# Optimization experiments

Hardware: AMD Instinct MI355X
Metric: run time of the kernel (lower is better)

Reference implementation:

```python
import jax, jax.numpy as jnp
import numpy as np

N_NODES = 50000
N_EDGES = 50000  # per-node attention scores are used as per-hyperedge weights => M == N
IN_CH = 128
OUT_CH = 128
NNZ = 800000


def setup_inputs() -> dict:
    key = jax.random.key(0)
    k = jax.random.split(key, 7)
    x = jax.random.normal(k[0], (N_NODES, IN_CH), dtype=jnp.float32)
    node_idx = jax.random.randint(k[1], (NNZ,), 0, N_NODES)
    edge_idx = jax.random.randint(k[2], (NNZ,), 0, N_EDGES)
    hyperedge_index = jnp.stack([node_idx, edge_idx]).astype(jnp.int64)
    s_in = 1.0 / np.sqrt(IN_CH)
    attn_w = jax.random.uniform(k[3], (1, IN_CH), minval=-s_in, maxval=s_in, dtype=jnp.float32)
    attn_b = jax.random.uniform(k[4], (1,), minval=-s_in, maxval=s_in, dtype=jnp.float32)
    lin_w = jax.random.uniform(k[5], (OUT_CH, IN_CH), minval=-s_in, maxval=s_in, dtype=jnp.float32)
    bias = jax.random.uniform(k[6], (OUT_CH,), minval=-s_in, maxval=s_in, dtype=jnp.float32)
    return {"x": x, "hyperedge_index": hyperedge_index,
            "attn_w": attn_w, "attn_b": attn_b, "lin_w": lin_w, "bias": bias}


def reference(x, hyperedge_index, attn_w, attn_b, lin_w, bias):
    # x: [N, C_in]; hyperedge_index: [2, nnz] (row 0: node ids, row 1: hyperedge ids)
    node_idx = hyperedge_index[0]
    edge_idx = hyperedge_index[1]
    N = x.shape[0]
    M = N_EDGES

    # edge_weight = sigmoid(attn(x)) -> used as hyperedge_weight (per-edge, M == N)
    w = jax.nn.sigmoid(x @ attn_w.T + attn_b)[:, 0]            # [M]

    xl = x @ lin_w.T                                           # [N, C_out]

    # D_v = sum of incident hyperedge weights per node; D^{-1} with inf -> 0
    D = jax.ops.segment_sum(w[edge_idx], node_idx, num_segments=N)
    Dinv = jnp.where(D > 0, 1.0 / D, 0.0)                      # [N]

    # B_e = hyperedge degree; B^{-1} with inf -> 0
    ones = jnp.ones(edge_idx.shape, dtype=x.dtype)
    Bdeg = jax.ops.segment_sum(ones, edge_idx, num_segments=M)
    Binv = jnp.where(Bdeg > 0, 1.0 / Bdeg, 0.0)                # [M]

    # node -> hyperedge: message = B_e^{-1} * x_j, aggregated at edge e
    msg = Binv[edge_idx][:, None] * xl[node_idx]               # [nnz, C_out]
    e_feat = jax.ops.segment_sum(msg, edge_idx, num_segments=M)

    # hyperedge -> node: message = D_v^{-1} * e_feat, aggregated at node v
    out = jax.ops.segment_sum(e_feat[edge_idx], node_idx, num_segments=N)
    out = Dinv[:, None] * out

    return out + bias
```

## Files before the change

### kernel.cpp

```cpp
#include <hip/hip_runtime.h>
#include <math.h>

#define CH 128
#define CAP 64
#define RSB 9
#define RS  (1 << RSB)
#define CAPB 10240
#define PB 2048
#define SUB 16
#define IDS 32

typedef __attribute__((ext_vector_type(8))) short bf16x8;
typedef __attribute__((ext_vector_type(4))) float f32x4;

__device__ __forceinline__ unsigned short f2bf(float f) {
    union { float f; unsigned u; } v; v.f = f;
    unsigned r = v.u + 0x7FFF + ((v.u >> 16) & 1);
    return (unsigned short)(r >> 16);
}
__device__ __forceinline__ float bflo(unsigned u) {
    union { unsigned u; float f; } v; v.u = u << 16; return v.f;
}
__device__ __forceinline__ float bfhi(unsigned u) {
    union { unsigned u; float f; } v; v.u = u & 0xFFFF0000u; return v.f;
}
__device__ __forceinline__ unsigned pack2bf(float a, float b) {
    return (unsigned)f2bf(a) | ((unsigned)f2bf(b) << 16);
}

__global__ __launch_bounds__(256) void fused_main(const float* __restrict__ x,
                                                  const float* __restrict__ attn_w,
                                                  const float* __restrict__ attn_b,
                                                  const float* __restrict__ lw,
                                                  unsigned short* __restrict__ xl,
                                                  float* __restrict__ w,
                                                  int nStrips,
                                                  const int* __restrict__ nidx,
                                                  const int* __restrict__ eidx,
                                                  int* __restrict__ binCnt,
                                                  unsigned int* __restrict__ binData,
                                                  int nnz, int nbd, int SB) {
    __shared__ unsigned short wl[128 * 136];
    __shared__ float awl[128];
    if ((int)blockIdx.x < SB) {
        int* hist = (int*)wl;
        int* base = ((int*)wl) + 256;
        int nbt = 2 * nbd;
        for (int i = threadIdx.x; i < nbt; i += 256) hist[i] = 0;
        __syncthreads();
        int k0 = blockIdx.x * PB + threadIdx.x;
        int vv[8], ee[8], sE[8], sN[8];
#pragma unroll
        for (int u = 0; u < 8; ++u) {
            int k = k0 + u * 256;
            if (k < nnz) {
                int v = nidx[k], e = eidx[k];
                vv[u] = v; ee[u] = e;
                sE[u] = atomicAdd(&hist[e >> RSB], 1);
                sN[u] = atomicAdd(&hist[nbd + (v >> RSB)], 1);
            } else vv[u] = -1;
        }
        __syncthreads();
        for (int i = threadIdx.x; i < nbt; i += 256)
            if (hist[i]) base[i] = atomicAdd(&binCnt[i], hist[i]);
        __syncthreads();
#pragma unroll
        for (int u = 0; u < 8; ++u) {
            if (vv[u] < 0) continue;
            int bE = ee[u] >> RSB;
            int bN = nbd + (vv[u] >> RSB);
            int iE = min(base[bE] + sE[u], CAPB - 1);
            int iN = min(base[bN] + sN[u], CAPB - 1);
            binData[(size_t)bE * CAPB + iE] = ((unsigned)ee[u] << 16) | (unsigned)vv[u];
            binData[(size_t)bN * CAPB + iN] = ((unsigned)vv[u] << 16) | (unsigned)ee[u];
        }
        return;
    }
    int tid = threadIdx.x;
    for (int i = tid; i < 2048; i += 256) {
        float4 vlo = ((const float4*)lw)[2 * i];
        float4 vhi = ((const float4*)lw)[2 * i + 1];
        int4 dst;
        dst.x = (int)pack2bf(vlo.x, vlo.y);
        dst.y = (int)pack2bf(vlo.z, vlo.w);
        dst.z = (int)pack2bf(vhi.x, vhi.y);
        dst.w = (int)pack2bf(vhi.z, vhi.w);
        *(int4*)(wl + (i >> 4) * 136 + (i & 15) * 8) = dst;
    }
    if (tid < 128) awl[tid] = attn_w[tid];
    float ab = attn_b[0];
    __syncthreads();
    int gb = blockIdx.x - SB;
    int wid = (gb << 2) | (tid >> 6);
    int lane = tid & 63;
    int m = lane & 15, quad = lane >> 4;
    int nWaves = ((int)gridDim.x - SB) << 2;
    for (int s = wid; s < nStrips; s += nWaves) {
        int r0 = s << 4;
        const float* xr = x + (size_t)(r0 + m) * CH + quad * 8;
        float att = 0.f;
        bf16x8 a0, a1, a2, a3;
#define LOAD_FRAG(AFRAG, F)                                                   \
        {                                                                     \
            float4 lo = *(const float4*)(xr + (F) * 32);                      \
            float4 hi = *(const float4*)(xr + (F) * 32 + 4);                  \
            const float* ap = &awl[(F) * 32 + quad * 8];                      \
            att += lo.x * ap[0] + lo.y * ap[1] + lo.z * ap[2] + lo.w * ap[3]  \
                 + hi.x * ap[4] + hi.y * ap[5] + hi.z * ap[6] + hi.w * ap[7]; \
            union { int4 i; bf16x8 v; } pk;                                   \
            pk.i.x = (int)pack2bf(lo.x, lo.y);                                \
            pk.i.y = (int)pack2bf(lo.z, lo.w);                                \
            pk.i.z = (int)pack2bf(hi.x, hi.y);                                \
            pk.i.w = (int)pack2bf(hi.z, hi.w);                                \
            AFRAG = pk.v;                                                     \
        }
        LOAD_FRAG(a0, 0)
        LOAD_FRAG(a1, 1)
        LOAD_FRAG(a2, 2)
        LOAD_FRAG(a3, 3)
#undef LOAD_FRAG
        att += __shfl_xor(att, 16, 64);
        att += __shfl_xor(att, 32, 64);
        if (quad == 0) w[r0 + m] = 1.0f / (1.0f + expf(-(att + ab)));
        unsigned short* xrow = xl + (size_t)(r0 + m) * CH + quad * 4;
#pragma unroll
        for (int c0 = 0; c0 < 128; c0 += 16) {
            const unsigned short* wr = wl + (c0 + m) * 136 + quad * 8;
            f32x4 acc = {0.f, 0.f, 0.f, 0.f};
            acc = __builtin_amdgcn_mfma_f32_16x16x32_bf16(*(const bf16x8*)(wr),      a0, acc, 0, 0, 0);
            acc = __builtin_amdgcn_mfma_f32_16x16x32_bf16(*(const bf16x8*)(wr + 32), a1, acc, 0, 0, 0);
            acc = __builtin_amdgcn_mfma_f32_16x16x32_bf16(*(const bf16x8*)(wr + 64), a2, acc, 0, 0, 0);
            acc = __builtin_amdgcn_mfma_f32_16x16x32_bf16(*(const bf16x8*)(wr + 96), a3, acc, 0, 0, 0);
            uint2 o;
            o.x = pack2bf(acc[0], acc[1]);
            o.y = pack2bf(acc[2], acc[3]);
            *(uint2*)(xrow + c0) = o;
        }
    }
}

__global__ __launch_bounds__(512, 8) void edge_agg(const int* __restrict__ binCnt,
                                                   const unsigned int* __restrict__ binData,
                                                   const unsigned short* __restrict__ xl,
                                                   unsigned short* __restrict__ ef, int M) {
    __shared__ unsigned short bucket[IDS * CAP];
    __shared__ int cl[IDS];
    int cb = blockIdx.x >> 4;
    int sr = blockIdx.x & (SUB - 1);
    int idBase = (cb << RSB) + (sr << 5);
    if (threadIdx.x < IDS) cl[threadIdx.x] = 0;
    __syncthreads();
    int n = min(binCnt[cb], CAPB);
    const unsigned int* src = binData + (size_t)cb * CAPB;
#define SCAN1(E) { int lid = (int)((E) >> 16) - idBase;                        \
                   if ((unsigned)lid < IDS) {                                  \
                       int r = atomicAdd(&cl[lid], 1);                         \
                       bucket[(lid << 6) + min(r, CAP - 1)] =                  \
                           (unsigned short)((E) & 0xFFFFu); } }
    for (int i0 = (int)threadIdx.x << 2; i0 < n; i0 += 2048) {
        if (i0 + 4 <= n) {
            uint4 e4 = *(const uint4*)(src + i0);
            SCAN1(e4.x) SCAN1(e4.y) SCAN1(e4.z) SCAN1(e4.w)
        } else {
            for (int i = i0; i < n; ++i) { unsigned int e1 = src[i]; SCAN1(e1) }
        }
    }
    __syncthreads();
    int wid = threadIdx.x >> 6, lane = threadIdx.x & 63;
    int half = lane >> 5, hl = lane & 31;
    for (int li = wid; li < IDS; li += 8) {
        int gid = idBase + li;
        if (gid >= M) break;
        int deg = cl[li];
        int dl = min(deg, CAP);
        const unsigned short* col = bucket + (li << 6);
        float4 acc = {0.f, 0.f, 0.f, 0.f};
        int npair = dl >> 1;
        int j = 0;
#define ROW(MID) { uint2 u = *(const uint2*)(xl + (size_t)(MID) * CH + 4 * hl); \
                   acc.x += bflo(u.x); acc.y += bfhi(u.x);                      \
                   acc.z += bflo(u.y); acc.w += bfhi(u.y); }
        for (; j + 4 <= npair; j += 4) {
            int m0 = col[2 * j + half];
            int m1 = col[2 * j + 2 + half];
            int m2 = col[2 * j + 4 + half];
            int m3 = col[2 * j + 6 + half];
            ROW(m0) ROW(m1) ROW(m2) ROW(m3)
        }
        for (; j < npair; ++j) { int m0 = col[2 * j + half]; ROW(m0) }
        if ((dl & 1) && half == 0) { int m0 = col[dl - 1]; ROW(m0) }
#undef ROW
        acc.x += __shfl_xor(acc.x, 32, 64);
        acc.y += __shfl_xor(acc.y, 32, 64);
        acc.z += __shfl_xor(acc.z, 32, 64);
        acc.w += __shfl_xor(acc.w, 32, 64);
        if (half == 0) {
            float binv = deg > 0 ? 1.0f / (float)deg : 0.0f;
            uint2 o;
            o.x = pack2bf(acc.x * binv, acc.y * binv);
            o.y = pack2bf(acc.z * binv, acc.w * binv);
            *(uint2*)(ef + (size_t)gid * CH + 4 * hl) = o;
        }
    }
}

__global__ __launch_bounds__(512, 8) void node_agg(const int* __restrict__ binCnt,
                                                   const unsigned int* __restrict__ binData,
                                                   const unsigned short* __restrict__ ef,
                                                   const float* __restrict__ w,
                                                   const float* __restrict__ bias,
                                                   float* __restrict__ out, int N) {
    __shared__ unsigned short bucket[IDS * CAP];
    __shared__ int cl[IDS];
    int cb = blockIdx.x >> 4;
    int sr = blockIdx.x & (SUB - 1);
    int idBase = (cb << RSB) + (sr << 5);
    if (threadIdx.x < IDS) cl[threadIdx.x] = 0;
    __syncthreads();
    int n = min(binCnt[cb], CAPB);
    const unsigned int* src = binData + (size_t)cb * CAPB;
    for (int i0 = (int)threadIdx.x << 2; i0 < n; i0 += 2048) {
        if (i0 + 4 <= n) {
            uint4 e4 = *(const uint4*)(src + i0);
            SCAN1(e4.x) SCAN1(e4.y) SCAN1(e4.z) SCAN1(e4.w)
        } else {
            for (int i = i0; i < n; ++i) { unsigned int e1 = src[i]; SCAN1(e1) }
        }
    }
#undef SCAN1
    __syncthreads();
    int wid = threadIdx.x >> 6, lane = threadIdx.x & 63;
    int half = lane >> 5, hl = lane & 31;
    for (int li = wid; li < IDS; li += 8) {
        int gid = idBase + li;
        if (gid >= N) break;
        int deg = cl[li];
        int dl = min(deg, CAP);
        const unsigned short* col = bucket + (li << 6);
        float4 acc = {0.f, 0.f, 0.f, 0.f};
        float ds = 0.f;
        int npair = dl >> 1;
        int j = 0;
#define ROW(MID) { uint2 u = *(const uint2*)(ef + (size_t)(MID) * CH + 4 * hl); \
                   ds += w[MID];                                                \
                   acc.x += bflo(u.x); acc.y += bfhi(u.x);                      \
                   acc.z += bflo(u.y); acc.w += bfhi(u.y); }
        for (; j + 4 <= npair; j += 4) {
            int m0 = col[2 * j + half];
            int m1 = col[2 * j + 2 + half];
            int m2 = col[2 * j + 4 + half];
            int m3 = col[2 * j + 6 + half];
            ROW(m0) ROW(m1) ROW(m2) ROW(m3)
        }
        for (; j < npair; ++j) { int m0 = col[2 * j + half]; ROW(m0) }
        if ((dl & 1) && half == 0) { int m0 = col[dl - 1]; ROW(m0) }
#undef ROW
        acc.x += __shfl_xor(acc.x, 32, 64);
        acc.y += __shfl_xor(acc.y, 32, 64);
        acc.z += __shfl_xor(acc.z, 32, 64);
        acc.w += __shfl_xor(acc.w, 32, 64);
        ds    += __shfl_xor(ds,    32, 64);
        if (half == 0) {
            float dinv = ds > 0.f ? 1.0f / ds : 0.0f;
            float4 bi = *(const float4*)(bias + 4 * hl);
            float4 o;
            o.x = acc.x * dinv + bi.x;
            o.y = acc.y * dinv + bi.y;
            o.z = acc.z * dinv + bi.z;
            o.w = acc.w * dinv + bi.w;
            *(float4*)(out + (size_t)gid * CH + 4 * hl) = o;
        }
    }
}

extern "C" void kernel_launch(void* const* d_in, const int* in_sizes, int n_in,
                              void* d_out, int out_size, void* d_ws, size_t ws_size,
                              hipStream_t stream) {
    const float* x      = (const float*)d_in[0];
    const int*   hei    = (const int*)d_in[1];
    const float* attn_w = (const float*)d_in[2];
    const float* attn_b = (const float*)d_in[3];
    const float* lin_w  = (const float*)d_in[4];
    const float* bias   = (const float*)d_in[5];
    float* out = (float*)d_out;

    const int N   = in_sizes[0] / CH;
    const int nnz = in_sizes[1] / 2;
    const int* nidx = hei;
    const int* eidx = hei + nnz;

    unsigned short* efbf = (unsigned short*)d_ws;
    float*          w    = (float*)(efbf + (size_t)N * CH);
    unsigned int*   binData = (unsigned int*)(w + N);
    int nbd = (N + RS - 1) >> RSB;
    int*            binCnt  = (int*)(binData + (size_t)2 * nbd * CAPB);

    unsigned short* xlbf = (unsigned short*)out;

    hipMemsetAsync(binCnt, 0, (size_t)2 * nbd * sizeof(int), stream);

    int SB = (nnz + PB - 1) / PB;
    int nStrips = N / 16;
    int GB = (nStrips + 3) / 4;
    fused_main<<<SB + GB, 256, 0, stream>>>(x, attn_w, attn_b, lin_w, xlbf, w,
                                            nStrips, nidx, eidx, binCnt, binData,
                                            nnz, nbd, SB);

    edge_agg<<<nbd * SUB, 512, 0, stream>>>(binCnt, binData, xlbf, efbf, N);
    node_agg<<<nbd * SUB, 512, 0, stream>>>(binCnt + nbd,
                                            binData + (size_t)nbd * CAPB,
                                            efbf, w, bias, out, N);
}
```

Measured before the change: 179.0 us.

## Split bf16 feature matrices into 32-channel chunks and aggregate per chunk

Stores xl and edge features as four column chunks of 32 channels each, with each chunk laid out contiguously per row. Each aggregation block now handles one chunk for 128 ids, and each wave gathers 8 rows at a time with 8 lanes per row. The aim is a smaller working set per chunk that fits in cache better during the random gathers. In exchange, every block rescans the bin data once per chunk, and node_agg reads w redundantly in every chunk.

```diff
diff --git a/kernel.cpp b/kernel.cpp
--- a/kernel.cpp
+++ b/kernel.cpp
@@ -7,8 +7,9 @@
 #define RS  (1 << RSB)
 #define CAPB 10240
 #define PB 2048
-#define SUB 16
-#define IDS 32
+#define NCHUNK 4
+#define CSUB 4
+#define IDS 128
 
 typedef __attribute__((ext_vector_type(8))) short bf16x8;
 typedef __attribute__((ext_vector_type(4))) float f32x4;
@@ -95,6 +96,7 @@
     int lane = tid & 63;
     int m = lane & 15, quad = lane >> 4;
     int nWaves = ((int)gridDim.x - SB) << 2;
+    size_t cs = (size_t)nStrips * 16 * 32;
     for (int s = wid; s < nStrips; s += nWaves) {
         int r0 = s << 4;
         const float* xr = x + (size_t)(r0 + m) * CH + quad * 8;
@@ -122,7 +124,7 @@
         att += __shfl_xor(att, 16, 64);
         att += __shfl_xor(att, 32, 64);
         if (quad == 0) w[r0 + m] = 1.0f / (1.0f + expf(-(att + ab)));
-        unsigned short* xrow = xl + (size_t)(r0 + m) * CH + quad * 4;
+        unsigned short* ob = xl + (size_t)(r0 + m) * 32 + quad * 4;
 #pragma unroll
         for (int c0 = 0; c0 < 128; c0 += 16) {
             const unsigned short* wr = wl + (c0 + m) * 136 + quad * 8;
@@ -134,7 +136,7 @@
             uint2 o;
             o.x = pack2bf(acc[0], acc[1]);
             o.y = pack2bf(acc[2], acc[3]);
-            *(uint2*)(xrow + c0) = o;
+            *(uint2*)(ob + (size_t)(c0 >> 5) * cs + (c0 & 16)) = o;
         }
     }
 }
@@ -142,13 +144,17 @@
 __global__ __launch_bounds__(512, 8) void edge_agg(const int* __restrict__ binCnt,
                                                    const unsigned int* __restrict__ binData,
                                                    const unsigned short* __restrict__ xl,
-                                                   unsigned short* __restrict__ ef, int M) {
+                                                   unsigned short* __restrict__ ef,
+                                                   int M, int rows) {
     __shared__ unsigned short bucket[IDS * CAP];
     __shared__ int cl[IDS];
-    int cb = blockIdx.x >> 4;
-    int sr = blockIdx.x & (SUB - 1);
-    int idBase = (cb << RSB) + (sr << 5);
-    if (threadIdx.x < IDS) cl[threadIdx.x] = 0;
+    int bid = blockIdx.x;
+    int chunk = bid & (NCHUNK - 1);
+    int t = bid >> 2;
+    int cb = t >> 2;
+    int sr = t & (CSUB - 1);
+    int idBase = (cb << RSB) + (sr << 7);
+    for (int i = threadIdx.x; i < IDS; i += 512) cl[i] = 0;
     __syncthreads();
     int n = min(binCnt[cb], CAPB);
     const unsigned int* src = binData + (size_t)cb * CAPB;
@@ -166,8 +172,10 @@
         }
     }
     __syncthreads();
+    size_t cbase = (size_t)chunk * rows * 32;
     int wid = threadIdx.x >> 6, lane = threadIdx.x & 63;
-    int half = lane >> 5, hl = lane & 31;
+    int g = lane >> 3, gl = lane & 7;
+    const unsigned short* bse = xl + cbase + (gl << 2);
     for (int li = wid; li < IDS; li += 8) {
         int gid = idBase + li;
         if (gid >= M) break;
@@ -175,31 +183,33 @@
         int dl = min(deg, CAP);
         const unsigned short* col = bucket + (li << 6);
         float4 acc = {0.f, 0.f, 0.f, 0.f};
-        int npair = dl >> 1;
         int j = 0;
-#define ROW(MID) { uint2 u = *(const uint2*)(xl + (size_t)(MID) * CH + 4 * hl); \
-                   acc.x += bflo(u.x); acc.y += bfhi(u.x);                      \
-                   acc.z += bflo(u.y); acc.w += bfhi(u.y); }
-        for (; j + 4 <= npair; j += 4) {
-            int m0 = col[2 * j + half];
-            int m1 = col[2 * j + 2 + half];
-            int m2 = col[2 * j + 4 + half];
-            int m3 = col[2 * j + 6 + half];
-            ROW(m0) ROW(m1) ROW(m2) ROW(m3)
-        }
-        for (; j < npair; ++j) { int m0 = col[2 * j + half]; ROW(m0) }
-        if ((dl & 1) && half == 0) { int m0 = col[dl - 1]; ROW(m0) }
-#undef ROW
-        acc.x += __shfl_xor(acc.x, 32, 64);
-        acc.y += __shfl_xor(acc.y, 32, 64);
-        acc.z += __shfl_xor(acc.z, 32, 64);
-        acc.w += __shfl_xor(acc.w, 32, 64);
-        if (half == 0) {
+#define ROW2(M0, M1) { uint2 u0 = *(const uint2*)(bse + (size_t)(M0) * 32);     \
+                       uint2 u1 = *(const uint2*)(bse + (size_t)(M1) * 32);     \
+                       acc.x += bflo(u0.x) + bflo(u1.x);                        \
+                       acc.y += bfhi(u0.x) + bfhi(u1.x);                        \
+                       acc.z += bflo(u0.y) + bflo(u1.y);                        \
+                       acc.w += bfhi(u0.y) + bfhi(u1.y); }
+#define ROW1(M0)     { uint2 u0 = *(const uint2*)(bse + (size_t)(M0) * 32);     \
+                       acc.x += bflo(u0.x); acc.y += bfhi(u0.x);                \
+                       acc.z += bflo(u0.y); acc.w += bfhi(u0.y); }
+        for (; j + 16 <= dl; j += 16) { int m0 = col[j + g], m1 = col[j + 8 + g]; ROW2(m0, m1) }
+        if (j + 8 <= dl) { int m0 = col[j + g]; ROW1(m0) j += 8; }
+        { int rem = dl - j; if (g < rem) { int m0 = col[j + g]; ROW1(m0) } }
+#undef ROW2
+#undef ROW1
+        acc.x += __shfl_xor(acc.x, 8, 64);  acc.y += __shfl_xor(acc.y, 8, 64);
+        acc.z += __shfl_xor(acc.z, 8, 64);  acc.w += __shfl_xor(acc.w, 8, 64);
+        acc.x += __shfl_xor(acc.x, 16, 64); acc.y += __shfl_xor(acc.y, 16, 64);
+        acc.z += __shfl_xor(acc.z, 16, 64); acc.w += __shfl_xor(acc.w, 16, 64);
+        acc.x += __shfl_xor(acc.x, 32, 64); acc.y += __shfl_xor(acc.y, 32, 64);
+        acc.z += __shfl_xor(acc.z, 32, 64); acc.w += __shfl_xor(acc.w, 32, 64);
+        if (g == 0) {
             float binv = deg > 0 ? 1.0f / (float)deg : 0.0f;
             uint2 o;
             o.x = pack2bf(acc.x * binv, acc.y * binv);
             o.y = pack2bf(acc.z * binv, acc.w * binv);
-            *(uint2*)(ef + (size_t)gid * CH + 4 * hl) = o;
+            *(uint2*)(ef + cbase + (size_t)gid * 32 + (gl << 2)) = o;
         }
     }
 }
@@ -209,13 +219,17 @@
                                                    const unsigned short* __restrict__ ef,
                                                    const float* __restrict__ w,
                                                    const float* __restrict__ bias,
-                                                   float* __restrict__ out, int N) {
+                                                   float* __restrict__ out,
+                                                   int N, int rows) {
     __shared__ unsigned short bucket[IDS * CAP];
     __shared__ int cl[IDS];
-    int cb = blockIdx.x >> 4;
-    int sr = blockIdx.x & (SUB - 1);
-    int idBase = (cb << RSB) + (sr << 5);
-    if (threadIdx.x < IDS) cl[threadIdx.x] = 0;
+    int bid = blockIdx.x;
+    int chunk = bid & (NCHUNK - 1);
+    int t = bid >> 2;
+    int cb = t >> 2;
+    int sr = t & (CSUB - 1);
+    int idBase = (cb << RSB) + (sr << 7);
+    for (int i = threadIdx.x; i < IDS; i += 512) cl[i] = 0;
     __syncthreads();
     int n = min(binCnt[cb], CAPB);
     const unsigned int* src = binData + (size_t)cb * CAPB;
@@ -229,8 +243,10 @@
     }
 #undef SCAN1
     __syncthreads();
+    size_t cbase = (size_t)chunk * rows * 32;
     int wid = threadIdx.x >> 6, lane = threadIdx.x & 63;
-    int half = lane >> 5, hl = lane & 31;
+    int g = lane >> 3, gl = lane & 7;
+    const unsigned short* bse = ef + cbase + (gl << 2);
     for (int li = wid; li < IDS; li += 8) {
         int gid = idBase + li;
         if (gid >= N) break;
@@ -239,36 +255,41 @@
         const unsigned short* col = bucket + (li << 6);
         float4 acc = {0.f, 0.f, 0.f, 0.f};
         float ds = 0.f;
-        int npair = dl >> 1;
         int j = 0;
-#define ROW(MID) { uint2 u = *(const uint2*)(ef + (size_t)(MID) * CH + 4 * hl); \
-                   ds += w[MID];                                                \
-                   acc.x += bflo(u.x); acc.y += bfhi(u.x);                      \
-                   acc.z += bflo(u.y); acc.w += bfhi(u.y); }
-        for (; j + 4 <= npair; j += 4) {
-            int m0 = col[2 * j + half];
-            int m1 = col[2 * j + 2 + half];
-            int m2 = col[2 * j + 4 + half];
-            int m3 = col[2 * j + 6 + half];
-            ROW(m0) ROW(m1) ROW(m2) ROW(m3)
-        }
-        for (; j < npair; ++j) { int m0 = col[2 * j + half]; ROW(m0) }
-        if ((dl & 1) && half == 0) { int m0 = col[dl - 1]; ROW(m0) }
-#undef ROW
-        acc.x += __shfl_xor(acc.x, 32, 64);
-        acc.y += __shfl_xor(acc.y, 32, 64);
-        acc.z += __shfl_xor(acc.z, 32, 64);
-        acc.w += __shfl_xor(acc.w, 32, 64);
-        ds    += __shfl_xor(ds,    32, 64);
-        if (half == 0) {
+#define ROW2(M0, M1) { uint2 u0 = *(const uint2*)(bse + (size_t)(M0) * 32);     \
+                       uint2 u1 = *(const uint2*)(bse + (size_t)(M1) * 32);     \
+                       ds += w[M0] + w[M1];                                     \
+                       acc.x += bflo(u0.x) + bflo(u1.x);                        \
+                       acc.y += bfhi(u0.x) + bfhi(u1.x);                        \
+                       acc.z += bflo(u0.y) + bflo(u1.y);                        \
+                       acc.w += bfhi(u0.y) + bfhi(u1.y); }
+#define ROW1(M0)     { uint2 u0 = *(const uint2*)(bse + (size_t)(M0) * 32);     \
+                       ds += w[M0];                                             \
+                       acc.x += bflo(u0.x); acc.y += bfhi(u0.x);                \
+                       acc.z += bflo(u0.y); acc.w += bfhi(u0.y); }
+        for (; j + 16 <= dl; j += 16) { int m0 = col[j + g], m1 = col[j + 8 + g]; ROW2(m0, m1) }
+        if (j + 8 <= dl) { int m0 = col[j + g]; ROW1(m0) j += 8; }
+        { int rem = dl - j; if (g < rem) { int m0 = col[j + g]; ROW1(m0) } }
+#undef ROW2
+#undef ROW1
+        acc.x += __shfl_xor(acc.x, 8, 64);  acc.y += __shfl_xor(acc.y, 8, 64);
+        acc.z += __shfl_xor(acc.z, 8, 64);  acc.w += __shfl_xor(acc.w, 8, 64);
+        ds    += __shfl_xor(ds, 8, 64);
+        acc.x += __shfl_xor(acc.x, 16, 64); acc.y += __shfl_xor(acc.y, 16, 64);
+        acc.z += __shfl_xor(acc.z, 16, 64); acc.w += __shfl_xor(acc.w, 16, 64);
+        ds    += __shfl_xor(ds, 16, 64);
+        acc.x += __shfl_xor(acc.x, 32, 64); acc.y += __shfl_xor(acc.y, 32, 64);
+        acc.z += __shfl_xor(acc.z, 32, 64); acc.w += __shfl_xor(acc.w, 32, 64);
+        ds    += __shfl_xor(ds, 32, 64);
+        if (g == 0) {
             float dinv = ds > 0.f ? 1.0f / ds : 0.0f;
-            float4 bi = *(const float4*)(bias + 4 * hl);
+            float4 bi = *(const float4*)(bias + chunk * 32 + (gl << 2));
             float4 o;
             o.x = acc.x * dinv + bi.x;
             o.y = acc.y * dinv + bi.y;
             o.z = acc.z * dinv + bi.z;
             o.w = acc.w * dinv + bi.w;
-            *(float4*)(out + (size_t)gid * CH + 4 * hl) = o;
+            *(float4*)(out + (size_t)gid * CH + chunk * 32 + (gl << 2)) = o;
         }
     }
 }
@@ -306,8 +327,9 @@
                                             nStrips, nidx, eidx, binCnt, binData,
                                             nnz, nbd, SB);
 
-    edge_agg<<<nbd * SUB, 512, 0, stream>>>(binCnt, binData, xlbf, efbf, N);
-    node_agg<<<nbd * SUB, 512, 0, stream>>>(binCnt + nbd,
-                                            binData + (size_t)nbd * CAPB,
-                                            efbf, w, bias, out, N);
-}
+    int aggGrid = nbd * CSUB * NCHUNK;
+    edge_agg<<<aggGrid, 512, 0, stream>>>(binCnt, binData, xlbf, efbf, N, N);
+    node_agg<<<aggGrid, 512, 0, stream>>>(binCnt + nbd,
+                                          binData + (size_t)nbd * CAPB,
+                                          efbf, w, bias, out, N, N);
+}
```

Result: slower. 217.0 us (+21.3%).
